# Kernel optimization log

Measured on AMD Instinct MI355X. Metric: run time of the kernel, lower is better.

Reference implementation:

```python
import jax, jax.numpy as jnp
import numpy as np

B, C, H, W = 4, 256, 64, 64
CH = C // 2  # inner channels of the non-local block


def _conv1x1(x, w, b):
    # 1x1 conv == channel-mixing einsum; x: [B,C,H,W], w: [O,C], b: [O]
    return jnp.einsum('oc,bchw->bohw', w, x) + b[None, :, None, None]


def setup_inputs() -> dict:
    key = jax.random.key(0)
    ks = jax.random.split(key, 9)
    s = 0.02  # small init so exp(scores) stays in fp32 range (no max-subtraction in this block)
    return {
        'x':  jax.random.normal(ks[0], (B, C, H, W), dtype=jnp.float32),
        'w1': s * jax.random.normal(ks[1], (CH, C), dtype=jnp.float32),
        'b1': jnp.zeros((CH,), jnp.float32),
        'w2': s * jax.random.normal(ks[2], (CH, C), dtype=jnp.float32),
        'b2': jnp.zeros((CH,), jnp.float32),
        'w3': s * jax.random.normal(ks[3], (CH, C), dtype=jnp.float32),
        'b3': jnp.zeros((CH,), jnp.float32),
        'w4': s * jax.random.normal(ks[4], (C, CH), dtype=jnp.float32),
        'b4': jnp.zeros((C,), jnp.float32),
    }


def reference(x, w1, b1, w2, b2, w3, b3, w4, b4):
    b, c, h, w = x.shape
    n = h * w
    theta = _conv1x1(x, w1, b1).reshape(b, -1, n)  # [B, C/2, N]
    phi   = _conv1x1(x, w2, b2).reshape(b, -1, n)  # [B, C/2, N]
    g     = _conv1x1(x, w3, b3).reshape(b, -1, n)  # [B, C/2, N]
    # full non-local affinity: [B, N, N]
    scores = jnp.einsum('bci,bcj->bij', theta, phi)
    attn = jnp.exp(scores)  # faithful: no max-subtraction in the original
    attn = attn / jnp.sum(attn, axis=1, keepdims=True)  # normalize over dim=1 as written
    y = jnp.einsum('bij,bcj->bci', attn, g)  # [B, C/2, N]
    y = y.reshape(b, -1, h, w)               # [B, C/2, H, W]
    out = _conv1x1(y, w4, b4) + x            # project back to C, residual
    return out
```

## Files before the change

### kernel.cpp

```cpp
#include <hip/hip_runtime.h>

#define DEVI __device__ __forceinline__

typedef __attribute__((ext_vector_type(8))) short bf16x8;
typedef __attribute__((ext_vector_type(4))) short bf16x4;
typedef __attribute__((ext_vector_type(4))) float f32x4;

#define MFMA16 __builtin_amdgcn_mfma_f32_16x16x32_bf16

DEVI short f2bs(float f) {
  union { float f; unsigned u; } v; v.f = f;
  unsigned r = v.u + 0x7fffu + ((v.u >> 16) & 1u);
  return (short)(r >> 16);
}
DEVI float bs2f(short s) {
  union { unsigned u; float f; } v; v.u = ((unsigned)(unsigned short)s) << 16;
  return v.f;
}

DEVI void gload_lds16(const short* g, short* lds) {
  __builtin_amdgcn_global_load_lds(
      (const __attribute__((address_space(1))) unsigned int*)g,
      (__attribute__((address_space(3))) unsigned int*)lds, 16, 0, 0);
}

DEVI void stage_chunk(short* lds, const short* g, int ldg, int tid) {
#pragma unroll
  for (int it = 0; it < 2; ++it) {
    int slot = it * 256 + tid;
    int row  = slot >> 2;
    int ko   = (slot & 3) << 3;
    gload_lds16(g + (size_t)row * ldg + ko, lds + slot * 8);
  }
}

DEVI void stage_chunk64(short* lds, const short* g, int ldg, int tid) {
  int row = tid >> 2, ko = (tid & 3) << 3;
  gload_lds16(g + (size_t)row * ldg + ko, lds + tid * 8);
}

DEVI bf16x8 lds8(const short* p) { return *(const bf16x8*)p; }

DEVI void zero_acc(f32x4 (&a)[4][4]) {
  f32x4 z = {0.f, 0.f, 0.f, 0.f};
#pragma unroll
  for (int i = 0; i < 4; ++i)
#pragma unroll
    for (int j = 0; j < 4; ++j) a[i][j] = z;
}

__global__ __launch_bounds__(256) void k_prep(const float* __restrict__ x,
                                              const float* __restrict__ w1,
                                              const float* __restrict__ w2,
                                              const float* __restrict__ w3,
                                              short* __restrict__ xt,
                                              short* __restrict__ w123) {
  int tid = threadIdx.x;
  if (blockIdx.y == 4) {
    int lin = blockIdx.z * 64 + blockIdx.x;
    for (int i = lin * 256 + tid; i < 384 * 256; i += 65536) {
      int r = i >> 8;
      const float* w = (r < 128) ? w1 : (r < 256 ? w2 : w3);
      w123[i] = f2bs(w[(size_t)(r & 127) * 256 + (i & 255)]);
    }
    return;
  }
  __shared__ float t[64][65];
  int b = blockIdx.z;
  int c0 = blockIdx.y * 64;
  int p0 = blockIdx.x * 64;
  const float* xb = x + (size_t)b * 256 * 4096;
#pragma unroll
  for (int i = 0; i < 16; ++i) {
    int idx = i * 256 + tid;
    int c = idx >> 6, p = idx & 63;
    t[p][c] = xb[(size_t)(c0 + c) * 4096 + p0 + p];
  }
  __syncthreads();
  short* xtb = xt + ((size_t)b * 4096 + p0) * 256 + c0;
#pragma unroll
  for (int i = 0; i < 16; ++i) {
    int idx = i * 256 + tid;
    int p = idx >> 6, c = idx & 63;
    xtb[(size_t)p * 256 + c] = f2bs(t[p][c]);
  }
}

__global__ __launch_bounds__(256) void k_proj(const short* __restrict__ xt,
                                              const short* __restrict__ w123,
                                              const float* __restrict__ b1,
                                              const float* __restrict__ b2,
                                              const float* __restrict__ b3,
                                              short* __restrict__ theta,
                                              short* __restrict__ phi,
                                              short* __restrict__ gT) {
  __shared__ short Lp[17408];
  int tid = threadIdx.x;
  int m0 = blockIdx.x * 128;
  int nb = blockIdx.y;
  int b  = blockIdx.z;
  int lane = tid & 63, wid = tid >> 6;
  int col = lane & 15, quad = lane >> 4;
  int wm = (wid >> 1) * 64, wn = (wid & 1) * 64;
  const short* A = xt + ((size_t)b * 4096 + m0) * 256;
  const short* B = w123 + (size_t)nb * 128 * 256;
  short* a0 = Lp;           short* b0 = Lp + 4096;
  short* a1 = Lp + 8192;    short* b1_ = Lp + 12288;
  stage_chunk(a0, A, 256, tid);
  stage_chunk(b0, B, 256, tid);
  f32x4 acc[4][4];
  zero_acc(acc);
  for (int ks = 0; ks < 8; ++ks) {
    short* ac = (ks & 1) ? a1 : a0;
    short* an = (ks & 1) ? a0 : a1;
    short* bc = (ks & 1) ? b1_ : b0;
    short* bn = (ks & 1) ? b0 : b1_;
    __syncthreads();
    if (ks < 7) {
      stage_chunk(an, A + (ks + 1) * 32, 256, tid);
      stage_chunk(bn, B + (ks + 1) * 32, 256, tid);
    }
    bf16x8 af[4], bf_[4];
#pragma unroll
    for (int mi = 0; mi < 4; ++mi) af[mi] = lds8(&ac[(wm + mi * 16 + col) * 32 + quad * 8]);
#pragma unroll
    for (int ni = 0; ni < 4; ++ni) bf_[ni] = lds8(&bc[(wn + ni * 16 + col) * 32 + quad * 8]);
#pragma unroll
    for (int mi = 0; mi < 4; ++mi)
#pragma unroll
      for (int ni = 0; ni < 4; ++ni)
        acc[mi][ni] = MFMA16(af[mi], bf_[ni], acc[mi][ni], 0, 0, 0);
  }
  const float* bias = (nb == 0) ? b1 : (nb == 1 ? b2 : b3);
  __syncthreads();
  short* oL = Lp;
  if (nb < 2) {
#pragma unroll
    for (int mi = 0; mi < 4; ++mi)
#pragma unroll
      for (int ni = 0; ni < 4; ++ni) {
        float bv = bias[wn + ni * 16 + col];
#pragma unroll
        for (int r = 0; r < 4; ++r)
          oL[(wm + mi * 16 + quad * 4 + r) * 136 + wn + ni * 16 + col] = f2bs(acc[mi][ni][r] + bv);
      }
    __syncthreads();
    short* O = ((nb == 0) ? theta : phi) + ((size_t)b * 4096 + m0) * 128;
#pragma unroll
    for (int it = 0; it < 8; ++it) {
      int slot = it * 256 + tid;
      int r = slot >> 4, cp = (slot & 15) * 8;
      *(bf16x8*)(O + (size_t)r * 128 + cp) = lds8(&oL[r * 136 + cp]);
    }
  } else {
#pragma unroll
    for (int mi = 0; mi < 4; ++mi)
#pragma unroll
      for (int ni = 0; ni < 4; ++ni) {
        float bv = bias[wn + ni * 16 + col];
#pragma unroll
        for (int r = 0; r < 4; ++r)
          oL[(wn + ni * 16 + col) * 136 + wm + mi * 16 + quad * 4 + r] = f2bs(acc[mi][ni][r] + bv);
      }
    __syncthreads();
    short* O = gT + (size_t)b * 128 * 4096 + m0;
#pragma unroll
    for (int it = 0; it < 8; ++it) {
      int slot = it * 256 + tid;
      int c = slot >> 4, p8 = (slot & 15) * 8;
      *(bf16x8*)(O + (size_t)c * 4096 + p8) = lds8(&oL[c * 136 + p8]);
    }
  }
}

__global__ __launch_bounds__(256, 2) void k_denom(const short* __restrict__ theta,
                                                  const short* __restrict__ phi,
                                                  float* __restrict__ dpart) {
  __shared__ short L[16384];
  __shared__ float part[128];
  int tid = threadIdx.x;
  int ib = blockIdx.x, jc = blockIdx.y, b = blockIdx.z;
  int lane = tid & 63, wid = tid >> 6;
  int col = lane & 15, quad = lane >> 4;
  int wmj = (wid & 1) * 32;
  int wni = (wid >> 1) * 64;
  const short* TH = theta + ((size_t)b * 4096 + ib * 128) * 128;
  const short* PH = phi + ((size_t)b * 4096 + (size_t)jc * 1024) * 128;
  float* D = dpart + ((size_t)(b * 32 + ib)) * 4096 + jc * 1024;
#pragma unroll
  for (int ks = 0; ks < 4; ++ks) stage_chunk(L + ks * 4096, TH + ks * 32, 128, tid);
  __syncthreads();
  bf16x8 bth[4][4];
#pragma unroll
  for (int ks = 0; ks < 4; ++ks)
#pragma unroll
    for (int ni = 0; ni < 4; ++ni)
      bth[ks][ni] = lds8(&L[ks * 4096 + (wni + ni * 16 + col) * 32 + quad * 8]);
  __syncthreads();
#pragma unroll
  for (int ks = 0; ks < 4; ++ks) stage_chunk64(L + ks * 2048, PH + ks * 32, 128, tid);
  for (int jt = 0; jt < 16; ++jt) {
    short* phc = L + (jt & 1) * 8192;
    short* phn = L + ((jt & 1) ^ 1) * 8192;
    __syncthreads();
    if (jt < 15) {
      const short* PHn = PH + (size_t)(jt + 1) * 64 * 128;
#pragma unroll
      for (int ks = 0; ks < 4; ++ks) stage_chunk64(phn + ks * 2048, PHn + ks * 32, 128, tid);
    }
    f32x4 s[2][4];
#pragma unroll
    for (int mi = 0; mi < 2; ++mi)
#pragma unroll
      for (int ni = 0; ni < 4; ++ni) s[mi][ni] = (f32x4){0.f, 0.f, 0.f, 0.f};
#pragma unroll
    for (int ks = 0; ks < 4; ++ks) {
      bf16x8 ap[2];
#pragma unroll
      for (int mi = 0; mi < 2; ++mi) ap[mi] = lds8(&phc[ks * 2048 + (wmj + mi * 16 + col) * 32 + quad * 8]);
#pragma unroll
      for (int mi = 0; mi < 2; ++mi)
#pragma unroll
        for (int ni = 0; ni < 4; ++ni)
          s[mi][ni] = MFMA16(ap[mi], bth[ks][ni], s[mi][ni], 0, 0, 0);
    }
#pragma unroll
    for (int mi = 0; mi < 2; ++mi)
#pragma unroll
      for (int r = 0; r < 4; ++r) {
        float ps = __expf(s[mi][0][r]) + __expf(s[mi][1][r]) +
                   __expf(s[mi][2][r]) + __expf(s[mi][3][r]);
        ps += __shfl_xor(ps, 1, 16);
        ps += __shfl_xor(ps, 2, 16);
        ps += __shfl_xor(ps, 4, 16);
        ps += __shfl_xor(ps, 8, 16);
        if (col == 0) part[(wid >> 1) * 64 + wmj + mi * 16 + quad * 4 + r] = ps;
      }
    __syncthreads();
    if (tid < 64) D[jt * 64 + tid] = part[tid] + part[64 + tid];
  }
}

__global__ __launch_bounds__(256, 2) void k_attn(const short* __restrict__ theta,
                                                 const short* __restrict__ phi,
                                                 const short* __restrict__ gT,
                                                 const float* __restrict__ dpart,
                                                 short* __restrict__ ypart) {
  __shared__ short L[35328];
  int tid = threadIdx.x;
  int ib = blockIdx.x, jc = blockIdx.y, b = blockIdx.z;
  int lane = tid & 63, wid = tid >> 6;
  int col = lane & 15, quad = lane >> 4;
  int wmj = (wid & 1) * 32;
  int wni = (wid >> 1) * 64;
  int wmi = (wid >> 1) * 64;
  int wnc = (wid & 1) * 64;
  const short* TH = theta + ((size_t)b * 4096 + ib * 128) * 128;
  const short* PH = phi + ((size_t)b * 4096 + (size_t)jc * 1024) * 128;
  const short* GT = gT + (size_t)b * 128 * 4096 + jc * 1024;
  short* ph = L;
  short* gp0 = L + 8192;
  short* gp1 = L + 16384;
  short* pP = L + 24576;
  float* dinv = (float*)(L + 33280);
  {
    int j4 = tid * 4;
    f32x4 ds = {0.f, 0.f, 0.f, 0.f};
    for (int ibb = 0; ibb < 32; ++ibb)
      ds += *(const f32x4*)(dpart + ((size_t)(b * 32 + ibb)) * 4096 + jc * 1024 + j4);
    f32x4 di;
#pragma unroll
    for (int e = 0; e < 4; ++e) di[e] = 1.0f / ds[e];
    *(f32x4*)(dinv + j4) = di;
  }
#pragma unroll
  for (int ks = 0; ks < 4; ++ks) stage_chunk(L + ks * 4096, TH + ks * 32, 128, tid);
  __syncthreads();
  bf16x8 bth[4][4];
#pragma unroll
  for (int ks = 0; ks < 4; ++ks)
#pragma unroll
    for (int ni = 0; ni < 4; ++ni)
      bth[ks][ni] = lds8(&L[ks * 4096 + (wni + ni * 16 + col) * 32 + quad * 8]);
  __syncthreads();
#pragma unroll
  for (int ks = 0; ks < 4; ++ks) stage_chunk64(ph + ks * 2048, PH + ks * 32, 128, tid);
#pragma unroll
  for (int s = 0; s < 2; ++s) stage_chunk(gp0 + s * 4096, GT + s * 32, 4096, tid);
  f32x4 accy[4][4];
  zero_acc(accy);
  for (int jt = 0; jt < 16; ++jt) {
    short* gpc = (jt & 1) ? gp1 : gp0;
    short* gpn = (jt & 1) ? gp0 : gp1;
    __syncthreads();
    f32x4 dv[2];
#pragma unroll
    for (int mi = 0; mi < 2; ++mi)
      dv[mi] = *(const f32x4*)(dinv + jt * 64 + wmj + mi * 16 + quad * 4);
    f32x4 s[2][4];
#pragma unroll
    for (int mi = 0; mi < 2; ++mi)
#pragma unroll
      for (int ni = 0; ni < 4; ++ni) s[mi][ni] = (f32x4){0.f, 0.f, 0.f, 0.f};
#pragma unroll
    for (int ks = 0; ks < 4; ++ks) {
      bf16x8 ap[2];
#pragma unroll
      for (int mi = 0; mi < 2; ++mi) ap[mi] = lds8(&ph[ks * 2048 + (wmj + mi * 16 + col) * 32 + quad * 8]);
#pragma unroll
      for (int mi = 0; mi < 2; ++mi)
#pragma unroll
        for (int ni = 0; ni < 4; ++ni)
          s[mi][ni] = MFMA16(ap[mi], bth[ks][ni], s[mi][ni], 0, 0, 0);
    }
#pragma unroll
    for (int mi = 0; mi < 2; ++mi) {
      int j0 = wmj + mi * 16 + quad * 4;
#pragma unroll
      for (int ni = 0; ni < 4; ++ni) {
        int i = wni + ni * 16 + col;
        bf16x4 pv;
#pragma unroll
        for (int r = 0; r < 4; ++r) pv[r] = f2bs(__expf(s[mi][ni][r]) * dv[mi][r]);
        *(bf16x4*)(pP + i * 68 + j0) = pv;
      }
    }
    __syncthreads();
    if (jt < 15) {
      const short* PHn = PH + (size_t)(jt + 1) * 64 * 128;
#pragma unroll
      for (int ks = 0; ks < 4; ++ks) stage_chunk64(ph + ks * 2048, PHn + ks * 32, 128, tid);
      const short* GTn = GT + (jt + 1) * 64;
#pragma unroll
      for (int s2 = 0; s2 < 2; ++s2) stage_chunk(gpn + s2 * 4096, GTn + s2 * 32, 4096, tid);
    }
#pragma unroll
    for (int ksj = 0; ksj < 2; ++ksj) {
      bf16x8 ap2[4], bg[4];
#pragma unroll
      for (int mi = 0; mi < 4; ++mi) ap2[mi] = lds8(&pP[(wmi + mi * 16 + col) * 68 + ksj * 32 + quad * 8]);
#pragma unroll
      for (int ni = 0; ni < 4; ++ni) bg[ni] = lds8(&gpc[ksj * 4096 + (wnc + ni * 16 + col) * 32 + quad * 8]);
#pragma unroll
      for (int mi = 0; mi < 4; ++mi)
#pragma unroll
        for (int ni = 0; ni < 4; ++ni)
          accy[mi][ni] = MFMA16(ap2[mi], bg[ni], accy[mi][ni], 0, 0, 0);
    }
  }
  short* Yp = ypart + ((size_t)(jc * 4 + b) * 4096 + (size_t)ib * 128) * 128;
#pragma unroll
  for (int half = 0; half < 2; ++half) {
    __syncthreads();
    if ((wid >> 1) == half) {
#pragma unroll
      for (int mi = 0; mi < 4; ++mi)
#pragma unroll
        for (int ni = 0; ni < 4; ++ni)
#pragma unroll
          for (int r = 0; r < 4; ++r)
            pP[(mi * 16 + quad * 4 + r) * 128 + wnc + ni * 16 + col] = f2bs(accy[mi][ni][r]);
    }
    __syncthreads();
#pragma unroll
    for (int it = 0; it < 4; ++it) {
      int slot = it * 256 + tid;
      int r = slot >> 4, c8 = (slot & 15) * 8;
      *(bf16x8*)(Yp + (size_t)(half * 64 + r) * 128 + c8) = lds8(&pP[r * 128 + c8]);
    }
  }
}

__global__ __launch_bounds__(256) void k_out(const short* __restrict__ ypart,
                                             const float* __restrict__ w4,
                                             const float* __restrict__ b4,
                                             const float* __restrict__ x,
                                             float* __restrict__ out) {
  __shared__ short wL[4 * 4096];
  __shared__ short yL[4 * 4096];
  __shared__ float bLs[128];
  int tid = threadIdx.x;
  int ibk = blockIdx.x, ob = blockIdx.y, b = blockIdx.z;
  int o0 = ob * 128, i0 = ibk * 128;
  int lane = tid & 63, wid = tid >> 6;
  int col = lane & 15, quad = lane >> 4;
  int wm = (wid >> 1) * 64, wn = (wid & 1) * 64;
#pragma unroll
  for (int it = 0; it < 16; ++it) {
    int slot = it * 256 + tid;
    int r = slot >> 5, c4 = (slot & 31) * 4;
    int ks = c4 >> 5, cr = c4 & 31;
    f32x4 wv = *(const f32x4*)(w4 + (size_t)(o0 + r) * 128 + c4);
    bf16x4 wp;
#pragma unroll
    for (int e = 0; e < 4; ++e) wp[e] = f2bs(wv[e]);
    *(bf16x4*)&wL[ks * 4096 + r * 32 + cr] = wp;
  }
#pragma unroll
  for (int it = 0; it < 8; ++it) {
    int slot = it * 256 + tid;
    int r = slot >> 4, c8 = (slot & 15) * 8;
    int ks = c8 >> 5, cr = c8 & 31;
    float a8[8];
#pragma unroll
    for (int e = 0; e < 8; ++e) a8[e] = 0.f;
#pragma unroll
    for (int p = 0; p < 4; ++p) {
      bf16x8 v = *(const bf16x8*)(ypart + ((size_t)(p * 4 + b) * 4096 + i0 + r) * 128 + c8);
#pragma unroll
      for (int e = 0; e < 8; ++e) a8[e] += bs2f(v[e]);
    }
    bf16x8 yv;
#pragma unroll
    for (int e = 0; e < 8; ++e) yv[e] = f2bs(a8[e]);
    *(bf16x8*)&yL[ks * 4096 + r * 32 + cr] = yv;
  }
  if (tid < 128) bLs[tid] = b4[o0 + tid];
  __syncthreads();
  f32x4 acc[4][4];
  zero_acc(acc);
#pragma unroll
  for (int ks = 0; ks < 4; ++ks) {
    bf16x8 af[4], bf_[4];
#pragma unroll
    for (int mi = 0; mi < 4; ++mi) af[mi] = lds8(&wL[ks * 4096 + (wm + mi * 16 + col) * 32 + quad * 8]);
#pragma unroll
    for (int ni = 0; ni < 4; ++ni) bf_[ni] = lds8(&yL[ks * 4096 + (wn + ni * 16 + col) * 32 + quad * 8]);
#pragma unroll
    for (int mi = 0; mi < 4; ++mi)
#pragma unroll
      for (int ni = 0; ni < 4; ++ni)
        acc[mi][ni] = MFMA16(af[mi], bf_[ni], acc[mi][ni], 0, 0, 0);
  }
  const float* X = x + ((size_t)b * 256 + o0) * 4096 + i0;
  float* O = out + ((size_t)b * 256 + o0) * 4096 + i0;
#pragma unroll
  for (int mi = 0; mi < 4; ++mi)
#pragma unroll
    for (int ni = 0; ni < 4; ++ni)
#pragma unroll
      for (int r = 0; r < 4; ++r) {
        int o = wm + mi * 16 + quad * 4 + r;
        int i = wn + ni * 16 + col;
        O[(size_t)o * 4096 + i] = acc[mi][ni][r] + X[(size_t)o * 4096 + i] + bLs[o];
      }
}

extern "C" void kernel_launch(void* const* d_in, const int* in_sizes, int n_in,
                              void* d_out, int out_size, void* d_ws, size_t ws_size,
                              hipStream_t stream) {
  const float* x  = (const float*)d_in[0];
  const float* w1 = (const float*)d_in[1];
  const float* b1 = (const float*)d_in[2];
  const float* w2 = (const float*)d_in[3];
  const float* b2 = (const float*)d_in[4];
  const float* w3 = (const float*)d_in[5];
  const float* b3 = (const float*)d_in[6];
  const float* w4 = (const float*)d_in[7];
  const float* b4 = (const float*)d_in[8];
  char* ws = (char*)d_ws;
  short* xt    = (short*)(ws + 0);
  short* w123  = (short*)(ws + 8388608);
  short* theta = (short*)(ws + 8585216);
  short* phi   = (short*)(ws + 12779520);
  short* gT    = (short*)(ws + 16973824);
  float* dpart = (float*)(ws + 21168128);
  short* ypart = (short*)(ws + 23265280);
  float* out   = (float*)d_out;
  (void)in_sizes; (void)n_in; (void)out_size; (void)ws_size;

  k_prep<<<dim3(64, 5, 4), dim3(256), 0, stream>>>(x, w1, w2, w3, xt, w123);
  k_proj<<<dim3(32, 3, 4), dim3(256), 0, stream>>>(xt, w123, b1, b2, b3, theta, phi, gT);
  k_denom<<<dim3(32, 4, 4), dim3(256), 0, stream>>>(theta, phi, dpart);
  k_attn<<<dim3(32, 4, 4), dim3(256), 0, stream>>>(theta, phi, gT, dpart, ypart);
  k_out<<<dim3(32, 2, 4), dim3(256), 0, stream>>>(ypart, w4, b4, x, out);
}
```

Baseline: 202.1 us.

## Double-buffer phi tiles, swizzle P layout, and hoist denominator reduction to kernel

```diff
diff --git a/kernel.cpp b/kernel.cpp
--- a/kernel.cpp
+++ b/kernel.cpp
@@ -241,38 +241,37 @@
   }
 }
 
+__global__ __launch_bounds__(256) void k_dred(const float* __restrict__ dpart,
+                                              float* __restrict__ dinv) {
+  int b = blockIdx.x >> 2, jb = blockIdx.x & 3;
+  int j4 = jb * 1024 + threadIdx.x * 4;
+  f32x4 s = {0.f, 0.f, 0.f, 0.f};
+  for (int ib = 0; ib < 32; ++ib)
+    s += *(const f32x4*)(dpart + ((size_t)(b * 32 + ib)) * 4096 + j4);
+  f32x4 r;
+#pragma unroll
+  for (int e = 0; e < 4; ++e) r[e] = 1.0f / s[e];
+  *(f32x4*)(dinv + (size_t)b * 4096 + j4) = r;
+}
+
 __global__ __launch_bounds__(256, 2) void k_attn(const short* __restrict__ theta,
                                                  const short* __restrict__ phi,
                                                  const short* __restrict__ gT,
-                                                 const float* __restrict__ dpart,
+                                                 const float* __restrict__ dinv,
                                                  short* __restrict__ ypart) {
-  __shared__ short L[35328];
+  __shared__ short L[40960];
   int tid = threadIdx.x;
   int ib = blockIdx.x, jc = blockIdx.y, b = blockIdx.z;
   int lane = tid & 63, wid = tid >> 6;
   int col = lane & 15, quad = lane >> 4;
   int wmj = (wid & 1) * 32;
   int wni = (wid >> 1) * 64;
-  int wmi = (wid >> 1) * 64;
   int wnc = (wid & 1) * 64;
   const short* TH = theta + ((size_t)b * 4096 + ib * 128) * 128;
   const short* PH = phi + ((size_t)b * 4096 + (size_t)jc * 1024) * 128;
   const short* GT = gT + (size_t)b * 128 * 4096 + jc * 1024;
-  short* ph = L;
-  short* gp0 = L + 8192;
-  short* gp1 = L + 16384;
-  short* pP = L + 24576;
-  float* dinv = (float*)(L + 33280);
-  {
-    int j4 = tid * 4;
-    f32x4 ds = {0.f, 0.f, 0.f, 0.f};
-    for (int ibb = 0; ibb < 32; ++ibb)
-      ds += *(const f32x4*)(dpart + ((size_t)(b * 32 + ibb)) * 4096 + jc * 1024 + j4);
-    f32x4 di;
-#pragma unroll
-    for (int e = 0; e < 4; ++e) di[e] = 1.0f / ds[e];
-    *(f32x4*)(dinv + j4) = di;
-  }
+  const float* DI = dinv + (size_t)b * 4096 + jc * 1024;
+  short* pP = L + 32768;
 #pragma unroll
   for (int ks = 0; ks < 4; ++ks) stage_chunk(L + ks * 4096, TH + ks * 32, 128, tid);
   __syncthreads();
@@ -284,19 +283,27 @@
       bth[ks][ni] = lds8(&L[ks * 4096 + (wni + ni * 16 + col) * 32 + quad * 8]);
   __syncthreads();
 #pragma unroll
-  for (int ks = 0; ks < 4; ++ks) stage_chunk64(ph + ks * 2048, PH + ks * 32, 128, tid);
-#pragma unroll
-  for (int s = 0; s < 2; ++s) stage_chunk(gp0 + s * 4096, GT + s * 32, 4096, tid);
+  for (int ks = 0; ks < 4; ++ks) stage_chunk64(L + ks * 2048, PH + ks * 32, 128, tid);
+#pragma unroll
+  for (int s = 0; s < 2; ++s) stage_chunk(L + 16384 + s * 4096, GT + s * 32, 4096, tid);
   f32x4 accy[4][4];
   zero_acc(accy);
   for (int jt = 0; jt < 16; ++jt) {
-    short* gpc = (jt & 1) ? gp1 : gp0;
-    short* gpn = (jt & 1) ? gp0 : gp1;
-    __syncthreads();
+    int cur = jt & 1;
+    short* phc = L + cur * 8192;
+    short* phn = L + (cur ^ 1) * 8192;
+    short* gpc = L + 16384 + cur * 8192;
+    short* gpn = L + 16384 + (cur ^ 1) * 8192;
+    __syncthreads();
+    if (jt < 15) {
+      const short* PHn = PH + (size_t)(jt + 1) * 64 * 128;
+#pragma unroll
+      for (int ks = 0; ks < 4; ++ks) stage_chunk64(phn + ks * 2048, PHn + ks * 32, 128, tid);
+    }
     f32x4 dv[2];
 #pragma unroll
     for (int mi = 0; mi < 2; ++mi)
-      dv[mi] = *(const f32x4*)(dinv + jt * 64 + wmj + mi * 16 + quad * 4);
+      dv[mi] = *(const f32x4*)(DI + jt * 64 + wmj + mi * 16 + quad * 4);
     f32x4 s[2][4];
 #pragma unroll
     for (int mi = 0; mi < 2; ++mi)
@@ -306,7 +313,7 @@
     for (int ks = 0; ks < 4; ++ks) {
       bf16x8 ap[2];
 #pragma unroll
-      for (int mi = 0; mi < 2; ++mi) ap[mi] = lds8(&ph[ks * 2048 + (wmj + mi * 16 + col) * 32 + quad * 8]);
+      for (int mi = 0; mi < 2; ++mi) ap[mi] = lds8(&phc[ks * 2048 + (wmj + mi * 16 + col) * 32 + quad * 8]);
 #pragma unroll
       for (int mi = 0; mi < 2; ++mi)
 #pragma unroll
@@ -316,20 +323,18 @@
 #pragma unroll
     for (int mi = 0; mi < 2; ++mi) {
       int j0 = wmj + mi * 16 + quad * 4;
+      int blk = j0 >> 3, off = j0 & 7;
 #pragma unroll
       for (int ni = 0; ni < 4; ++ni) {
         int i = wni + ni * 16 + col;
         bf16x4 pv;
 #pragma unroll
         for (int r = 0; r < 4; ++r) pv[r] = f2bs(__expf(s[mi][ni][r]) * dv[mi][r]);
-        *(bf16x4*)(pP + i * 68 + j0) = pv;
+        *(bf16x4*)(pP + i * 64 + ((blk ^ (i & 7)) << 3) + off) = pv;
       }
     }
     __syncthreads();
     if (jt < 15) {
-      const short* PHn = PH + (size_t)(jt + 1) * 64 * 128;
-#pragma unroll
-      for (int ks = 0; ks < 4; ++ks) stage_chunk64(ph + ks * 2048, PHn + ks * 32, 128, tid);
       const short* GTn = GT + (jt + 1) * 64;
 #pragma unroll
       for (int s2 = 0; s2 < 2; ++s2) stage_chunk(gpn + s2 * 4096, GTn + s2 * 32, 4096, tid);
@@ -338,7 +343,10 @@
     for (int ksj = 0; ksj < 2; ++ksj) {
       bf16x8 ap2[4], bg[4];
 #pragma unroll
-      for (int mi = 0; mi < 4; ++mi) ap2[mi] = lds8(&pP[(wmi + mi * 16 + col) * 68 + ksj * 32 + quad * 8]);
+      for (int mi = 0; mi < 4; ++mi) {
+        int i = wni + mi * 16 + col;
+        ap2[mi] = lds8(&pP[i * 64 + (((ksj * 4 + quad) ^ (i & 7)) << 3)]);
+      }
 #pragma unroll
       for (int ni = 0; ni < 4; ++ni) bg[ni] = lds8(&gpc[ksj * 4096 + (wnc + ni * 16 + col) * 32 + quad * 8]);
 #pragma unroll
@@ -465,13 +473,15 @@
   short* phi   = (short*)(ws + 12779520);
   short* gT    = (short*)(ws + 16973824);
   float* dpart = (float*)(ws + 21168128);
-  short* ypart = (short*)(ws + 23265280);
+  float* dinv  = (float*)(ws + 23265280);
+  short* ypart = (short*)(ws + 23330816);
   float* out   = (float*)d_out;
   (void)in_sizes; (void)n_in; (void)out_size; (void)ws_size;
 
   k_prep<<<dim3(64, 5, 4), dim3(256), 0, stream>>>(x, w1, w2, w3, xt, w123);
   k_proj<<<dim3(32, 3, 4), dim3(256), 0, stream>>>(xt, w123, b1, b2, b3, theta, phi, gT);
   k_denom<<<dim3(32, 4, 4), dim3(256), 0, stream>>>(theta, phi, dpart);
-  k_attn<<<dim3(32, 4, 4), dim3(256), 0, stream>>>(theta, phi, gT, dpart, ypart);
+  k_dred<<<dim3(16), dim3(256), 0, stream>>>(dpart, dinv);
+  k_attn<<<dim3(32, 4, 4), dim3(256), 0, stream>>>(theta, phi, gT, dinv, ypart);
   k_out<<<dim3(32, 2, 4), dim3(256), 0, stream>>>(ypart, w4, b4, x, out);
 }
```

Measured after the change: 187.7 us. 1.08x faster.
